# Performance work log

Measured on AMD Instinct MI355X. Metric: run time of the kernel, lower is better.

Reference implementation:

```python
import jax, jax.numpy as jnp
import numpy as np

HIDDEN = 512
LAYERS = 2
MAX_ROLLOUT = 12
STATE_SIZE = [8, 6, 4, 1]
ANCHOR = 64
BATCH = 1024
BLOCK_N = len(STATE_SIZE)


def setup_inputs() -> dict:
    key = jax.random.key(0)
    ks = jax.random.split(key, 20)
    s = 0.05
    d = {}
    d["x0"] = jax.random.normal(ks[0], (1, BATCH, HIDDEN), jnp.float32)
    d["lstm_Wih"] = jax.random.normal(ks[1], (LAYERS, 4 * HIDDEN, HIDDEN), jnp.float32) * s
    d["lstm_Whh"] = jax.random.normal(ks[2], (LAYERS, 4 * HIDDEN, HIDDEN), jnp.float32) * s
    d["lstm_bih"] = jax.random.normal(ks[3], (LAYERS, 4 * HIDDEN), jnp.float32) * s
    d["lstm_bhh"] = jax.random.normal(ks[4], (LAYERS, 4 * HIDDEN), jnp.float32) * s
    d["Wc0"] = jax.random.normal(ks[5], (STATE_SIZE[0], HIDDEN), jnp.float32) * s
    d["bc0"] = jax.random.normal(ks[6], (STATE_SIZE[0],), jnp.float32) * s
    d["Wc1"] = jax.random.normal(ks[7], (STATE_SIZE[1], HIDDEN), jnp.float32) * s
    d["bc1"] = jax.random.normal(ks[8], (STATE_SIZE[1],), jnp.float32) * s
    d["Wc2"] = jax.random.normal(ks[9], (STATE_SIZE[2], HIDDEN), jnp.float32) * s
    d["bc2"] = jax.random.normal(ks[10], (STATE_SIZE[2],), jnp.float32) * s
    d["Wprev"] = jax.random.normal(ks[11], (ANCHOR, HIDDEN), jnp.float32) * s
    d["bprev"] = jax.random.normal(ks[12], (ANCHOR,), jnp.float32) * s
    d["Wcurr"] = jax.random.normal(ks[13], (ANCHOR, HIDDEN), jnp.float32) * s
    d["bcurr"] = jax.random.normal(ks[14], (ANCHOR,), jnp.float32) * s
    d["Wanc"] = jax.random.normal(ks[15], (HIDDEN, MAX_ROLLOUT - 1), jnp.float32) * s
    d["banc"] = jax.random.normal(ks[16], (HIDDEN,), jnp.float32) * s
    d["v"] = jax.random.normal(ks[17], (ANCHOR,), jnp.float32)
    d["batch_size"] = BATCH
    return d


def _lstm_step(x, h, c, Wih, Whh, bih, bhh):
    # x: [B,H]; h,c: [L,B,H]; multi-layer LSTM, torch gate order (i,f,g,o)
    hs, cs = [], []
    inp = x
    for l in range(LAYERS):
        g = inp @ Wih[l].T + h[l] @ Whh[l].T + bih[l] + bhh[l]  # [B,4H]
        gi, gf, gg, go = jnp.split(g, 4, axis=-1)
        cl = jax.nn.sigmoid(gf) * c[l] + jax.nn.sigmoid(gi) * jnp.tanh(gg)
        hl = jax.nn.sigmoid(go) * jnp.tanh(cl)
        hs.append(hl)
        cs.append(cl)
        inp = hl
    return inp, jnp.stack(hs), jnp.stack(cs)


def _forward(x0, lstm_Wih, lstm_Whh, lstm_bih, lstm_bhh, Wc0, bc0, Wc1, bc1, Wc2, bc2,
             Wprev, bprev, Wcurr, bcurr, Wanc, banc, v, batch_size):
    Wcls = [Wc0, Wc1, Wc2]
    bcls = [bc0, bc1, bc2]
    B = batch_size
    anchor_hs = [jnp.zeros((B, HIDDEN), x0.dtype)]
    inp = x0[0]  # [B,H]
    h = jnp.zeros((LAYERS, B, HIDDEN), x0.dtype)
    c = jnp.zeros((LAYERS, B, HIDDEN), x0.dtype)
    outputs = []
    for i in range(MAX_ROLLOUT * BLOCK_N):
        state_idx = i % BLOCK_N
        cycle_idx = i // BLOCK_N
        out, h, c = _lstm_step(inp, h, c, lstm_Wih, lstm_Whh, lstm_bih, lstm_bhh)
        if state_idx < BLOCK_N - 1:
            logit = out @ Wcls[state_idx].T + bcls[state_idx]
            outputs.append(jax.nn.softmax(logit, axis=-1))  # [B, STATE_SIZE[state_idx]]
            # note: `inp` is NOT updated on classifier steps, matching the original
        else:
            anchor_hs.append(out)
            if cycle_idx == 0:
                anchor_o = jnp.zeros((B, MAX_ROLLOUT - 1), x0.dtype)
            else:
                # attention over anchor_hs[0:cycle_idx] (zeros + previous cycles),
                # exactly as the original indexes after appending current out
                prev = jnp.stack(anchor_hs[:cycle_idx])  # [cyc, B, H]
                t = jnp.tanh(prev @ Wprev.T + bprev + (out @ Wcurr.T + bcurr)[None])  # [cyc,B,A]
                scores = jax.nn.sigmoid(jnp.einsum('a,cba->cb', v, t))  # [cyc, B]
                anchor_o = jnp.pad(scores.T, ((0, 0), (0, MAX_ROLLOUT - cycle_idx - 1)))
            outputs.append(anchor_o)  # [B, MAX_ROLLOUT-1]
            inp = anchor_o @ Wanc.T + banc  # anchor_embedding feeds next step
    # outputs are [B, S_i] / [B, MAX_ROLLOUT-1]; concat into a single [B, 348] tensor
    return jnp.concatenate(outputs, axis=1)


def reference(x0, lstm_Wih, lstm_Whh, lstm_bih, lstm_bhh, Wc0, bc0, Wc1, bc1, Wc2, bc2,
              Wprev, bprev, Wcurr, bcurr, Wanc, banc, v, batch_size):
    return _forward(x0, lstm_Wih, lstm_Whh, lstm_bih, lstm_bhh, Wc0, bc0, Wc1, bc1, Wc2, bc2,
                    Wprev, bprev, Wcurr, bcurr, Wanc, banc, v, batch_size)
```

## Files before the change

kernel.cpp:

```cpp
#include <hip/hip_runtime.h>
#include <hip/hip_bf16.h>

#define BATCH 1024
#define HID   512
#define OUTW  348
#define BK    64

using short8 = __attribute__((ext_vector_type(8))) short;
using bf16x8 = __attribute__((ext_vector_type(8))) __bf16;
using f32x4  = __attribute__((ext_vector_type(4))) float;

__device__ __forceinline__ float bf2f(unsigned short u) {
  union { unsigned int i; float f; } x; x.i = ((unsigned int)u) << 16; return x.f;
}
__device__ __forceinline__ unsigned short f2bf(float f) {
  __hip_bfloat16 b = __float2bfloat16(f);
  return __builtin_bit_cast(unsigned short, b);
}
__device__ __forceinline__ float sigm(float x) { return 1.0f / (1.0f + __expf(-x)); }

__device__ __forceinline__ f32x4 mfma_bf16(short8 a, short8 b, f32x4 c) {
  return __builtin_amdgcn_mfma_f32_16x16x32_bf16(
      __builtin_bit_cast(bf16x8, a), __builtin_bit_cast(bf16x8, b), c, 0, 0, 0);
}

typedef const __attribute__((address_space(1))) unsigned int* gas_p;
typedef __attribute__((address_space(3))) unsigned int* las_p;
__device__ __forceinline__ void gload16(const void* g, void* l) {
  __builtin_amdgcn_global_load_lds((gas_p)g, (las_p)l, 16, 0, 0);
}


__global__ void k_convert(const float* __restrict__ src, unsigned short* __restrict__ dst, int n) {
  int i = (blockIdx.x * blockDim.x + threadIdx.x) * 4;
  if (i + 3 < n) {
    float4 v = *(const float4*)(src + i);
    dst[i + 0] = f2bf(v.x); dst[i + 1] = f2bf(v.y);
    dst[i + 2] = f2bf(v.z); dst[i + 3] = f2bf(v.w);
  } else {
    for (int j = 0; j < 4 && i + j < n; ++j) dst[i + j] = f2bf(src[i + j]);
  }
}

__global__ void k_wqp(const float* __restrict__ Wcurr, const float* __restrict__ Wprev,
                      unsigned short* __restrict__ dst) {
  int i = blockIdx.x * blockDim.x + threadIdx.x;
  int row = i >> 9, col = i & 511;
  float v = (row < 64) ? Wcurr[row * 512 + col] : Wprev[(row - 64) * 512 + col];
  dst[i] = f2bf(v);
}

__global__ void k_bias(const float* __restrict__ bih, const float* __restrict__ bhh,
                       float* __restrict__ bsum) {
  int i = blockIdx.x * blockDim.x + threadIdx.x;
  if (i < 4096) bsum[i] = bih[i] + bhh[i];
}

__global__ void k_zero(uint4* __restrict__ p, int n16) {
  int i = blockIdx.x * blockDim.x + threadIdx.x;
  if (i < n16) p[i] = make_uint4(0u, 0u, 0u, 0u);
}

__global__ void k_p0(float* __restrict__ P, const float* __restrict__ bprev) {
  int i = blockIdx.x * blockDim.x + threadIdx.x;
  P[i] = bprev[i & 63];
}

__global__ __launch_bounds__(256) void k_gates(
    const unsigned short* __restrict__ Xin,
    const unsigned short* __restrict__ Hprev,
    const unsigned short* __restrict__ Wih,
    const unsigned short* __restrict__ Whh,
    const float* __restrict__ bias,
    float* __restrict__ C,
    unsigned short* __restrict__ Hout)
{
  __shared__ unsigned short Ab[2][4096];
  __shared__ unsigned short Bb[2][4096];
  const int w = threadIdx.x >> 6, lane = threadIdx.x & 63;
  const int m0 = blockIdx.x * 64;
  const int n0 = blockIdx.y * 16;
  const int l16 = lane & 15, kg = lane >> 4;

  auto stage = [&](int kt, int buf) {
    const unsigned short* Asrc = (kt < 8) ? Xin : Hprev;
    const unsigned short* Wsrc = (kt < 8) ? Wih : Whh;
    const int k0 = (kt & 7) * BK;
#pragma unroll
    for (int j = 0; j < 2; ++j) {
      int s = w * 128 + j * 64 + lane;
      int row = s >> 3;
      int ke = ((s & 7) ^ (row & 7)) << 3;
      gload16(Asrc + (size_t)(m0 + row) * HID + k0 + ke, &Ab[buf][(w * 128 + j * 64) * 8]);
    }
#pragma unroll
    for (int j = 0; j < 2; ++j) {
      int s = w * 128 + j * 64 + lane;
      int fr = s >> 3;
      int g = fr >> 4, c = fr & 15;
      int ke = ((s & 7) ^ (fr & 7)) << 3;
      gload16(Wsrc + (size_t)(g * 512 + n0 + c) * HID + k0 + ke, &Bb[buf][(w * 128 + j * 64) * 8]);
    }
  };

  f32x4 acc[4];
#pragma unroll
  for (int g = 0; g < 4; ++g) acc[g] = (f32x4)(0.0f);

  stage(0, 0);
  for (int kt = 0; kt < 16; ++kt) {
    __syncthreads();
    if (kt < 15) stage(kt + 1, (kt + 1) & 1);
    const int buf = kt & 1;
#pragma unroll
    for (int ko = 0; ko < 2; ++ko) {
      const int acb = ko * 64 + kg * 16;
      const int ar = w * 16 + l16;
      short8 a = *(const short8*)&Ab[buf][ar * 64 + ((acb ^ ((ar & 7) << 4)) >> 1)];
#pragma unroll
      for (int g = 0; g < 4; ++g) {
        const int br = g * 16 + l16;
        short8 b = *(const short8*)&Bb[buf][br * 64 + ((acb ^ ((br & 7) << 4)) >> 1)];
        acc[g] = mfma_bf16(a, b, acc[g]);
      }
    }
  }

  const int ccol = n0 + l16;
  const int crow = m0 + w * 16 + kg * 4;
  const float b0 = bias[ccol], b1 = bias[512 + ccol];
  const float b2 = bias[1024 + ccol], b3 = bias[1536 + ccol];
#pragma unroll
  for (int r = 0; r < 4; ++r) {
    const int m = crow + r;
    float gi = acc[0][r] + b0;
    float gf = acc[1][r] + b1;
    float gg = acc[2][r] + b2;
    float go = acc[3][r] + b3;
    float cold = C[m * HID + ccol];
    float cn = sigm(gf) * cold + sigm(gi) * tanhf(gg);
    float hn = sigm(go) * tanhf(cn);
    C[m * HID + ccol] = cn;
    Hout[m * HID + ccol] = f2bf(hn);
  }
}

template <int S>
__global__ __launch_bounds__(256) void k_cls(const unsigned short* __restrict__ h1,
                                             const float* __restrict__ Wc,
                                             const float* __restrict__ bc,
                                             float* __restrict__ out, int obase) {
  const int wave = threadIdx.x >> 6, lane = threadIdx.x & 63;
  const int r = blockIdx.x * 4 + wave;
  short8 hv = *(const short8*)(h1 + r * HID + lane * 8);
  float hf[8];
#pragma unroll
  for (int j = 0; j < 8; ++j) hf[j] = bf2f((unsigned short)hv[j]);
  float logit[S];
#pragma unroll
  for (int s = 0; s < S; ++s) {
    const float* wr = Wc + s * HID + lane * 8;
    float p = 0.f;
#pragma unroll
    for (int j = 0; j < 8; ++j) p += hf[j] * wr[j];
#pragma unroll
    for (int off = 32; off; off >>= 1) p += __shfl_xor(p, off);
    logit[s] = p + bc[s];
  }
  if (lane == 0) {
    float m = logit[0];
#pragma unroll
    for (int s = 1; s < S; ++s) m = fmaxf(m, logit[s]);
    float e[S], den = 0.f;
#pragma unroll
    for (int s = 0; s < S; ++s) { e[s] = __expf(logit[s] - m); den += e[s]; }
    float inv = 1.0f / den;
#pragma unroll
    for (int s = 0; s < S; ++s) out[r * OUTW + obase + s] = e[s] * inv;
  }
}

__global__ __launch_bounds__(256) void k_qp(
    const unsigned short* __restrict__ h1,
    const unsigned short* __restrict__ Wqp,
    const float* __restrict__ bcurr, const float* __restrict__ bprev,
    float* __restrict__ Q,
    float* __restrict__ P,
    int cyc) {
  __shared__ unsigned short Ab[2][4096];
  __shared__ unsigned short Bb[2][1024];
  const int w = threadIdx.x >> 6, lane = threadIdx.x & 63;
  const int m0 = blockIdx.x * 64, n0 = blockIdx.y * 16;
  const int l16 = lane & 15, kg = lane >> 4;

  auto stage = [&](int kt, int buf) {
    const int k0 = kt * BK;
#pragma unroll
    for (int j = 0; j < 2; ++j) {
      int s = w * 128 + j * 64 + lane;
      int row = s >> 3;
      int ke = ((s & 7) ^ (row & 7)) << 3;
      gload16(h1 + (size_t)(m0 + row) * HID + k0 + ke, &Ab[buf][(w * 128 + j * 64) * 8]);
    }
    if (w < 2) {
      int s = w * 64 + lane;
      int row = s >> 3;
      int ke = ((s & 7) ^ (row & 7)) << 3;
      gload16(Wqp + (size_t)(n0 + row) * HID + k0 + ke, &Bb[buf][(w * 64) * 8]);
    }
  };

  f32x4 acc = (f32x4)(0.0f);
  stage(0, 0);
  for (int kt = 0; kt < 8; ++kt) {
    __syncthreads();
    if (kt < 7) stage(kt + 1, (kt + 1) & 1);
    const int buf = kt & 1;
#pragma unroll
    for (int ko = 0; ko < 2; ++ko) {
      const int acb = ko * 64 + kg * 16;
      const int ar = w * 16 + l16;
      short8 a = *(const short8*)&Ab[buf][ar * 64 + ((acb ^ ((ar & 7) << 4)) >> 1)];
      const int br = l16;
      short8 b = *(const short8*)&Bb[buf][br * 64 + ((acb ^ ((br & 7) << 4)) >> 1)];
      acc = mfma_bf16(a, b, acc);
    }
  }

  const int col = n0 + l16;
  const int r0 = m0 + w * 16 + kg * 4;
#pragma unroll
  for (int r = 0; r < 4; ++r) {
    const int m = r0 + r;
    float val = acc[r] + (col < 64 ? bcurr[col] : bprev[col - 64]);
    if (col < 64) Q[m * 64 + col] = val;
    else if (cyc + 1 < 12) P[(cyc + 1) * (BATCH * 64) + m * 64 + (col - 64)] = val;
  }
}

template <int CYC>
__global__ __launch_bounds__(256) void k_scores(
    const float* __restrict__ Q, const float* __restrict__ P,
    const float* __restrict__ vv, const float* __restrict__ Wanc,
    const float* __restrict__ banc, float* __restrict__ out,
    unsigned short* __restrict__ X) {
  const int w = threadIdx.x >> 6, lane = threadIdx.x & 63;
  const int r = blockIdx.x * 4 + w;
  const float q = Q[r * 64 + lane];
  const float vl = vv[lane];
  float sk[CYC > 0 ? CYC : 1];
#pragma unroll
  for (int k = 0; k < CYC; ++k) {
    float t = tanhf(P[k * (BATCH * 64) + r * 64 + lane] + q) * vl;
#pragma unroll
    for (int off = 32; off; off >>= 1) t += __shfl_xor(t, off);
    sk[k] = sigm(t);
  }
  float ov = 0.0f;
#pragma unroll
  for (int k = 0; k < 11; ++k)
    if (lane == k) ov = (k < CYC) ? sk[k] : 0.0f;
  if (lane < 11) out[r * OUTW + CYC * 29 + 18 + lane] = ov;

  const int d0 = lane * 8;
#pragma unroll
  for (int j = 0; j < 8; ++j) {
    const int d = d0 + j;
    float x = banc[d];
#pragma unroll
    for (int k = 0; k < CYC; ++k) x += sk[k] * Wanc[d * 11 + k];
    X[r * HID + d] = f2bf(x);
  }
}


extern "C" void kernel_launch(void* const* d_in, const int* in_sizes, int n_in,
                              void* d_out, int out_size, void* d_ws, size_t ws_size,
                              hipStream_t stream) {
  const float* x0    = (const float*)d_in[0];
  const float* lWih  = (const float*)d_in[1];
  const float* lWhh  = (const float*)d_in[2];
  const float* lbih  = (const float*)d_in[3];
  const float* lbhh  = (const float*)d_in[4];
  const float* Wc0   = (const float*)d_in[5];
  const float* bc0   = (const float*)d_in[6];
  const float* Wc1   = (const float*)d_in[7];
  const float* bc1   = (const float*)d_in[8];
  const float* Wc2   = (const float*)d_in[9];
  const float* bc2   = (const float*)d_in[10];
  const float* Wprev = (const float*)d_in[11];
  const float* bprev = (const float*)d_in[12];
  const float* Wcurr = (const float*)d_in[13];
  const float* bcurr = (const float*)d_in[14];
  const float* Wanc  = (const float*)d_in[15];
  const float* banc  = (const float*)d_in[16];
  const float* v     = (const float*)d_in[17];
  float* out = (float*)d_out;

  const size_t NW  = 2 * 2048 * 512;
  const size_t NBH = (size_t)BATCH * HID;

  char* ws = (char*)d_ws;
  size_t off = 0;
  auto alloc = [&](size_t bytes) { char* p = ws + off; off += (bytes + 255) & ~(size_t)255; return p; };
  unsigned short* Wih_b = (unsigned short*)alloc(NW * 2);
  unsigned short* Whh_b = (unsigned short*)alloc(NW * 2);
  unsigned short* Wqp_b = (unsigned short*)alloc(128 * 512 * 2);
  float*          biasS = (float*)alloc(4096 * 4);
  unsigned short* Xb    = (unsigned short*)alloc(NBH * 2);
  unsigned short* Hb0   = (unsigned short*)alloc(2 * NBH * 2);
  unsigned short* Hb1   = (unsigned short*)alloc(2 * NBH * 2);
  float*          C0    = (float*)alloc(NBH * 4);
  float*          C1    = (float*)alloc(NBH * 4);
  float*          P     = (float*)alloc((size_t)12 * BATCH * 64 * 4);
  float*          Qb    = (float*)alloc((size_t)BATCH * 64 * 4);

  k_convert<<<dim3((NW / 4 + 255) / 256), dim3(256), 0, stream>>>(lWih, Wih_b, (int)NW);
  k_convert<<<dim3((NW / 4 + 255) / 256), dim3(256), 0, stream>>>(lWhh, Whh_b, (int)NW);
  k_convert<<<dim3((NBH / 4 + 255) / 256), dim3(256), 0, stream>>>(x0, Xb, (int)NBH);
  k_wqp<<<dim3(256), dim3(256), 0, stream>>>(Wcurr, Wprev, Wqp_b);
  k_bias<<<dim3(16), dim3(256), 0, stream>>>(lbih, lbhh, biasS);
  {
    size_t zb = 2 * NBH * 2 + 2 * NBH * 2 + NBH * 4 + NBH * 4;
    int n16 = (int)(zb / 16);
    k_zero<<<dim3((n16 + 255) / 256), dim3(256), 0, stream>>>((uint4*)Hb0, n16);
  }
  k_p0<<<dim3(256), dim3(256), 0, stream>>>(P, bprev);

  for (int t = 0; t < 48; ++t) {
    const int rd = t & 1, wr = (t + 1) & 1;
    unsigned short* h0r = Hb0 + rd * NBH;
    unsigned short* h0w = Hb0 + wr * NBH;
    unsigned short* h1r = Hb1 + rd * NBH;
    unsigned short* h1w = Hb1 + wr * NBH;

    k_gates<<<dim3(16, 32), dim3(256), 0, stream>>>(Xb, h0r, Wih_b, Whh_b, biasS, C0, h0w);
    k_gates<<<dim3(16, 32), dim3(256), 0, stream>>>(h0w, h1r, Wih_b + 2048 * 512,
                                                    Whh_b + 2048 * 512, biasS + 2048, C1, h1w);
    const int st = t & 3, cyc = t >> 2, base = cyc * 29;
    if (st == 0)      k_cls<8><<<dim3(256), dim3(256), 0, stream>>>(h1w, Wc0, bc0, out, base);
    else if (st == 1) k_cls<6><<<dim3(256), dim3(256), 0, stream>>>(h1w, Wc1, bc1, out, base + 8);
    else if (st == 2) k_cls<4><<<dim3(256), dim3(256), 0, stream>>>(h1w, Wc2, bc2, out, base + 14);
    else {
      k_qp<<<dim3(16, 8), dim3(256), 0, stream>>>(h1w, Wqp_b, bcurr, bprev, Qb, P, cyc);
      switch (cyc) {
        case 0:  k_scores<0><<<dim3(256), dim3(256), 0, stream>>>(Qb, P, v, Wanc, banc, out, Xb); break;
        case 1:  k_scores<1><<<dim3(256), dim3(256), 0, stream>>>(Qb, P, v, Wanc, banc, out, Xb); break;
        case 2:  k_scores<2><<<dim3(256), dim3(256), 0, stream>>>(Qb, P, v, Wanc, banc, out, Xb); break;
        case 3:  k_scores<3><<<dim3(256), dim3(256), 0, stream>>>(Qb, P, v, Wanc, banc, out, Xb); break;
        case 4:  k_scores<4><<<dim3(256), dim3(256), 0, stream>>>(Qb, P, v, Wanc, banc, out, Xb); break;
        case 5:  k_scores<5><<<dim3(256), dim3(256), 0, stream>>>(Qb, P, v, Wanc, banc, out, Xb); break;
        case 6:  k_scores<6><<<dim3(256), dim3(256), 0, stream>>>(Qb, P, v, Wanc, banc, out, Xb); break;
        case 7:  k_scores<7><<<dim3(256), dim3(256), 0, stream>>>(Qb, P, v, Wanc, banc, out, Xb); break;
        case 8:  k_scores<8><<<dim3(256), dim3(256), 0, stream>>>(Qb, P, v, Wanc, banc, out, Xb); break;
        case 9:  k_scores<9><<<dim3(256), dim3(256), 0, stream>>>(Qb, P, v, Wanc, banc, out, Xb); break;
        case 10: k_scores<10><<<dim3(256), dim3(256), 0, stream>>>(Qb, P, v, Wanc, banc, out, Xb); break;
        default: k_scores<11><<<dim3(256), dim3(256), 0, stream>>>(Qb, P, v, Wanc, banc, out, Xb); break;
      }
    }
  }
  (void)in_sizes; (void)n_in; (void)out_size; (void)ws_size;
}
```

Baseline: 1.698 ms.

## Wavefront-fuse LSTM layer GEMMs across timesteps with larger tiles and fused classifiers

Replaces the per-layer gate kernels with a merged kernel that runs layer 1 at step t together with layer 0 at step t+1, plus the classifier head of the previous step, in one launch. The GEMM tile grows from 64x16 to 128x32 cells per block, with each wave computing a 4x4 grid of MFMA tiles, so operands are reused more per LDS load. Launch count and serialization between dependent kernels drop. The cost is fewer blocks per launch (128 per GEMM), higher register and LDS use, and more complex buffer indexing across timesteps.

```diff
diff --git a/kernel.cpp b/kernel.cpp
--- a/kernel.cpp
+++ b/kernel.cpp
@@ -4,7 +4,6 @@
 #define BATCH 1024
 #define HID   512
 #define OUTW  348
-#define BK    64
 
 using short8 = __attribute__((ext_vector_type(8))) short;
 using bf16x8 = __attribute__((ext_vector_type(8))) __bf16;
@@ -66,46 +65,55 @@
   P[i] = bprev[i & 63];
 }
 
-__global__ __launch_bounds__(256) void k_gates(
-    const unsigned short* __restrict__ Xin,
-    const unsigned short* __restrict__ Hprev,
-    const unsigned short* __restrict__ Wih,
-    const unsigned short* __restrict__ Whh,
-    const float* __restrict__ bias,
-    float* __restrict__ C,
-    unsigned short* __restrict__ Hout)
-{
-  __shared__ unsigned short Ab[2][4096];
-  __shared__ unsigned short Bb[2][4096];
-  const int w = threadIdx.x >> 6, lane = threadIdx.x & 63;
-  const int m0 = blockIdx.x * 64;
-  const int n0 = blockIdx.y * 16;
+
+struct GJob {
+  const unsigned short *X, *H, *Wih, *Whh;
+  const float *bias;
+  float *C;
+  unsigned short *Hout;
+};
+struct CJob {
+  const unsigned short* h;
+  const float *Wc, *bc;
+  float* out;
+  int obase;
+};
+
+__device__ __forceinline__ void run_gemm(const GJob& j, int lb,
+                                         unsigned short (*Ab)[8192],
+                                         unsigned short (*Bb)[8192]) {
+  const int tid = threadIdx.x, w = tid >> 6, lane = tid & 63;
+  const int wm = w & 1, wc = w >> 1;
+  const int mt = lb & 7, nt = lb >> 3;
+  const int m0 = mt * 128, n0 = nt * 32;
   const int l16 = lane & 15, kg = lane >> 4;
 
   auto stage = [&](int kt, int buf) {
-    const unsigned short* Asrc = (kt < 8) ? Xin : Hprev;
-    const unsigned short* Wsrc = (kt < 8) ? Wih : Whh;
-    const int k0 = (kt & 7) * BK;
-#pragma unroll
-    for (int j = 0; j < 2; ++j) {
-      int s = w * 128 + j * 64 + lane;
-      int row = s >> 3;
-      int ke = ((s & 7) ^ (row & 7)) << 3;
-      gload16(Asrc + (size_t)(m0 + row) * HID + k0 + ke, &Ab[buf][(w * 128 + j * 64) * 8]);
-    }
-#pragma unroll
-    for (int j = 0; j < 2; ++j) {
-      int s = w * 128 + j * 64 + lane;
-      int fr = s >> 3;
-      int g = fr >> 4, c = fr & 15;
-      int ke = ((s & 7) ^ (fr & 7)) << 3;
-      gload16(Wsrc + (size_t)(g * 512 + n0 + c) * HID + k0 + ke, &Bb[buf][(w * 128 + j * 64) * 8]);
+    const unsigned short* As = (kt < 8) ? j.X : j.H;
+    const unsigned short* Bs = (kt < 8) ? j.Wih : j.Whh;
+    const int k0 = (kt & 7) * 64;
+#pragma unroll
+    for (int i = 0; i < 4; ++i) {
+      int g = i * 256 + tid;
+      int row = g >> 3, cg = g & 7;
+      int ke = (cg ^ (row & 7)) << 3;
+      gload16(As + (size_t)(m0 + row) * HID + k0 + ke, &Ab[buf][g * 8]);
+    }
+#pragma unroll
+    for (int i = 0; i < 4; ++i) {
+      int g = i * 256 + tid;
+      int fr = g >> 3, cg = g & 7;
+      int gate = fr >> 5, cell = fr & 31;
+      int ke = (cg ^ (fr & 7)) << 3;
+      gload16(Bs + (size_t)(gate * HID + n0 + cell) * HID + k0 + ke, &Bb[buf][g * 8]);
     }
   };
 
-  f32x4 acc[4];
-#pragma unroll
-  for (int g = 0; g < 4; ++g) acc[g] = (f32x4)(0.0f);
+  f32x4 acc[4][4];
+#pragma unroll
+  for (int mi = 0; mi < 4; ++mi)
+#pragma unroll
+    for (int g = 0; g < 4; ++g) acc[mi][g] = (f32x4)(0.0f);
 
   stage(0, 0);
   for (int kt = 0; kt < 16; ++kt) {
@@ -115,68 +123,91 @@
 #pragma unroll
     for (int ko = 0; ko < 2; ++ko) {
       const int acb = ko * 64 + kg * 16;
-      const int ar = w * 16 + l16;
-      short8 a = *(const short8*)&Ab[buf][ar * 64 + ((acb ^ ((ar & 7) << 4)) >> 1)];
+      short8 a[4], b[4];
+#pragma unroll
+      for (int mi = 0; mi < 4; ++mi) {
+        const int r = wm * 64 + mi * 16 + l16;
+        a[mi] = *(const short8*)&Ab[buf][r * 64 + ((acb ^ ((r & 7) << 4)) >> 1)];
+      }
 #pragma unroll
       for (int g = 0; g < 4; ++g) {
-        const int br = g * 16 + l16;
-        short8 b = *(const short8*)&Bb[buf][br * 64 + ((acb ^ ((br & 7) << 4)) >> 1)];
-        acc[g] = mfma_bf16(a, b, acc[g]);
+        const int fr = g * 32 + wc * 16 + l16;
+        b[g] = *(const short8*)&Bb[buf][fr * 64 + ((acb ^ ((fr & 7) << 4)) >> 1)];
       }
-    }
-  }
-
-  const int ccol = n0 + l16;
-  const int crow = m0 + w * 16 + kg * 4;
-  const float b0 = bias[ccol], b1 = bias[512 + ccol];
-  const float b2 = bias[1024 + ccol], b3 = bias[1536 + ccol];
-#pragma unroll
-  for (int r = 0; r < 4; ++r) {
-    const int m = crow + r;
-    float gi = acc[0][r] + b0;
-    float gf = acc[1][r] + b1;
-    float gg = acc[2][r] + b2;
-    float go = acc[3][r] + b3;
-    float cold = C[m * HID + ccol];
-    float cn = sigm(gf) * cold + sigm(gi) * tanhf(gg);
-    float hn = sigm(go) * tanhf(cn);
-    C[m * HID + ccol] = cn;
-    Hout[m * HID + ccol] = f2bf(hn);
+#pragma unroll
+      for (int mi = 0; mi < 4; ++mi)
+#pragma unroll
+        for (int g = 0; g < 4; ++g) acc[mi][g] = mfma_bf16(a[mi], b[g], acc[mi][g]);
+    }
+  }
+
+  const int cell = n0 + wc * 16 + l16;
+  const float b0 = j.bias[cell], b1 = j.bias[512 + cell];
+  const float b2 = j.bias[1024 + cell], b3 = j.bias[1536 + cell];
+#pragma unroll
+  for (int mi = 0; mi < 4; ++mi) {
+#pragma unroll
+    for (int r = 0; r < 4; ++r) {
+      const int m = m0 + wm * 64 + mi * 16 + kg * 4 + r;
+      float gi = acc[mi][0][r] + b0;
+      float gf = acc[mi][1][r] + b1;
+      float gg = acc[mi][2][r] + b2;
+      float go = acc[mi][3][r] + b3;
+      float cold = j.C[m * HID + cell];
+      float cn = sigm(gf) * cold + sigm(gi) * tanhf(gg);
+      float hn = sigm(go) * tanhf(cn);
+      j.C[m * HID + cell] = cn;
+      j.Hout[m * HID + cell] = f2bf(hn);
+    }
   }
 }
 
 template <int S>
-__global__ __launch_bounds__(256) void k_cls(const unsigned short* __restrict__ h1,
-                                             const float* __restrict__ Wc,
-                                             const float* __restrict__ bc,
-                                             float* __restrict__ out, int obase) {
-  const int wave = threadIdx.x >> 6, lane = threadIdx.x & 63;
-  const int r = blockIdx.x * 4 + wave;
-  short8 hv = *(const short8*)(h1 + r * HID + lane * 8);
-  float hf[8];
-#pragma unroll
-  for (int j = 0; j < 8; ++j) hf[j] = bf2f((unsigned short)hv[j]);
-  float logit[S];
-#pragma unroll
-  for (int s = 0; s < S; ++s) {
-    const float* wr = Wc + s * HID + lane * 8;
-    float p = 0.f;
-#pragma unroll
-    for (int j = 0; j < 8; ++j) p += hf[j] * wr[j];
-#pragma unroll
-    for (int off = 32; off; off >>= 1) p += __shfl_xor(p, off);
-    logit[s] = p + bc[s];
-  }
-  if (lane == 0) {
-    float m = logit[0];
-#pragma unroll
-    for (int s = 1; s < S; ++s) m = fmaxf(m, logit[s]);
-    float e[S], den = 0.f;
-#pragma unroll
-    for (int s = 0; s < S; ++s) { e[s] = __expf(logit[s] - m); den += e[s]; }
-    float inv = 1.0f / den;
-#pragma unroll
-    for (int s = 0; s < S; ++s) out[r * OUTW + obase + s] = e[s] * inv;
+__device__ __forceinline__ void run_cls(const CJob& c, int cb) {
+  const int w = threadIdx.x >> 6, lane = threadIdx.x & 63;
+#pragma unroll
+  for (int i = 0; i < 8; ++i) {
+    const int r = (cb * 4 + w) * 8 + i;
+    short8 hv = *(const short8*)(c.h + r * HID + lane * 8);
+    float hf[8];
+#pragma unroll
+    for (int j = 0; j < 8; ++j) hf[j] = bf2f((unsigned short)hv[j]);
+    float logit[S];
+#pragma unroll
+    for (int s = 0; s < S; ++s) {
+      const float* wr = c.Wc + s * HID + lane * 8;
+      float p = 0.f;
+#pragma unroll
+      for (int j = 0; j < 8; ++j) p += hf[j] * wr[j];
+#pragma unroll
+      for (int off = 32; off; off >>= 1) p += __shfl_xor(p, off);
+      logit[s] = p + c.bc[s];
+    }
+    if (lane == 0) {
+      float m = logit[0];
+#pragma unroll
+      for (int s = 1; s < S; ++s) m = fmaxf(m, logit[s]);
+      float e[S], den = 0.f;
+#pragma unroll
+      for (int s = 0; s < S; ++s) { e[s] = __expf(logit[s] - m); den += e[s]; }
+      float inv = 1.0f / den;
+#pragma unroll
+      for (int s = 0; s < S; ++s) c.out[r * OUTW + c.obase + s] = e[s] * inv;
+    }
+  }
+}
+
+template <int S, bool HASB>
+__global__ __launch_bounds__(256, 2) void k_gates2(GJob A, GJob B, CJob C) {
+  __shared__ unsigned short Ab[2][8192];
+  __shared__ unsigned short Bb[2][8192];
+  const int b = blockIdx.x;
+  if (b < 128) {
+    run_gemm(A, b, Ab, Bb);
+  } else if (HASB && b < 256) {
+    run_gemm(B, b - 128, Ab, Bb);
+  } else {
+    if constexpr (S > 0) run_cls<S>(C, b - (HASB ? 256 : 128));
   }
 }
 
@@ -194,7 +225,7 @@
   const int l16 = lane & 15, kg = lane >> 4;
 
   auto stage = [&](int kt, int buf) {
-    const int k0 = kt * BK;
+    const int k0 = kt * 64;
 #pragma unroll
     for (int j = 0; j < 2; ++j) {
       int s = w * 128 + j * 64 + lane;
@@ -327,37 +358,50 @@
   }
   k_p0<<<dim3(256), dim3(256), 0, stream>>>(P, bprev);
 
-  for (int t = 0; t < 48; ++t) {
-    const int rd = t & 1, wr = (t + 1) & 1;
-    unsigned short* h0r = Hb0 + rd * NBH;
-    unsigned short* h0w = Hb0 + wr * NBH;
-    unsigned short* h1r = Hb1 + rd * NBH;
-    unsigned short* h1w = Hb1 + wr * NBH;
-
-    k_gates<<<dim3(16, 32), dim3(256), 0, stream>>>(Xb, h0r, Wih_b, Whh_b, biasS, C0, h0w);
-    k_gates<<<dim3(16, 32), dim3(256), 0, stream>>>(h0w, h1r, Wih_b + 2048 * 512,
-                                                    Whh_b + 2048 * 512, biasS + 2048, C1, h1w);
-    const int st = t & 3, cyc = t >> 2, base = cyc * 29;
-    if (st == 0)      k_cls<8><<<dim3(256), dim3(256), 0, stream>>>(h1w, Wc0, bc0, out, base);
-    else if (st == 1) k_cls<6><<<dim3(256), dim3(256), 0, stream>>>(h1w, Wc1, bc1, out, base + 8);
-    else if (st == 2) k_cls<4><<<dim3(256), dim3(256), 0, stream>>>(h1w, Wc2, bc2, out, base + 14);
-    else {
-      k_qp<<<dim3(16, 8), dim3(256), 0, stream>>>(h1w, Wqp_b, bcurr, bprev, Qb, P, cyc);
-      switch (cyc) {
-        case 0:  k_scores<0><<<dim3(256), dim3(256), 0, stream>>>(Qb, P, v, Wanc, banc, out, Xb); break;
-        case 1:  k_scores<1><<<dim3(256), dim3(256), 0, stream>>>(Qb, P, v, Wanc, banc, out, Xb); break;
-        case 2:  k_scores<2><<<dim3(256), dim3(256), 0, stream>>>(Qb, P, v, Wanc, banc, out, Xb); break;
-        case 3:  k_scores<3><<<dim3(256), dim3(256), 0, stream>>>(Qb, P, v, Wanc, banc, out, Xb); break;
-        case 4:  k_scores<4><<<dim3(256), dim3(256), 0, stream>>>(Qb, P, v, Wanc, banc, out, Xb); break;
-        case 5:  k_scores<5><<<dim3(256), dim3(256), 0, stream>>>(Qb, P, v, Wanc, banc, out, Xb); break;
-        case 6:  k_scores<6><<<dim3(256), dim3(256), 0, stream>>>(Qb, P, v, Wanc, banc, out, Xb); break;
-        case 7:  k_scores<7><<<dim3(256), dim3(256), 0, stream>>>(Qb, P, v, Wanc, banc, out, Xb); break;
-        case 8:  k_scores<8><<<dim3(256), dim3(256), 0, stream>>>(Qb, P, v, Wanc, banc, out, Xb); break;
-        case 9:  k_scores<9><<<dim3(256), dim3(256), 0, stream>>>(Qb, P, v, Wanc, banc, out, Xb); break;
-        case 10: k_scores<10><<<dim3(256), dim3(256), 0, stream>>>(Qb, P, v, Wanc, banc, out, Xb); break;
-        default: k_scores<11><<<dim3(256), dim3(256), 0, stream>>>(Qb, P, v, Wanc, banc, out, Xb); break;
-      }
-    }
+  auto jobL0 = [&](int u) {
+    GJob j; j.X = Xb; j.H = Hb0 + (u & 1) * NBH;
+    j.Wih = Wih_b; j.Whh = Whh_b; j.bias = biasS; j.C = C0;
+    j.Hout = Hb0 + ((u + 1) & 1) * NBH; return j;
+  };
+  auto jobL1 = [&](int t) {
+    GJob j; j.X = Hb0 + ((t + 1) & 1) * NBH; j.H = Hb1 + (t & 1) * NBH;
+    j.Wih = Wih_b + 2048 * 512; j.Whh = Whh_b + 2048 * 512; j.bias = biasS + 2048; j.C = C1;
+    j.Hout = Hb1 + ((t + 1) & 1) * NBH; return j;
+  };
+  auto h1of = [&](int t) { return (const unsigned short*)(Hb1 + ((t + 1) & 1) * NBH); };
+  GJob dummy{}; CJob nocls{};
+
+  k_gates2<0, false><<<dim3(128), dim3(256), 0, stream>>>(jobL0(0), dummy, nocls);
+
+  for (int c = 0; c < 12; ++c) {
+    const int t0 = 4 * c, t1 = t0 + 1, t2 = t0 + 2, t3 = t0 + 3;
+    const int base = c * 29;
+    CJob cls0{h1of(t0), Wc0, bc0, out, base};
+    CJob cls1{h1of(t1), Wc1, bc1, out, base + 8};
+    CJob cls2{h1of(t2), Wc2, bc2, out, base + 14};
+
+    k_gates2<0, true><<<dim3(256), dim3(256), 0, stream>>>(jobL1(t0), jobL0(t1), nocls);
+    k_gates2<8, true><<<dim3(288), dim3(256), 0, stream>>>(jobL1(t1), jobL0(t2), cls0);
+    k_gates2<6, true><<<dim3(288), dim3(256), 0, stream>>>(jobL1(t2), jobL0(t3), cls1);
+    k_gates2<4, false><<<dim3(160), dim3(256), 0, stream>>>(jobL1(t3), dummy, cls2);
+
+    k_qp<<<dim3(16, 8), dim3(256), 0, stream>>>(h1of(t3), Wqp_b, bcurr, bprev, Qb, P, c);
+    switch (c) {
+      case 0:  k_scores<0><<<dim3(256), dim3(256), 0, stream>>>(Qb, P, v, Wanc, banc, out, Xb); break;
+      case 1:  k_scores<1><<<dim3(256), dim3(256), 0, stream>>>(Qb, P, v, Wanc, banc, out, Xb); break;
+      case 2:  k_scores<2><<<dim3(256), dim3(256), 0, stream>>>(Qb, P, v, Wanc, banc, out, Xb); break;
+      case 3:  k_scores<3><<<dim3(256), dim3(256), 0, stream>>>(Qb, P, v, Wanc, banc, out, Xb); break;
+      case 4:  k_scores<4><<<dim3(256), dim3(256), 0, stream>>>(Qb, P, v, Wanc, banc, out, Xb); break;
+      case 5:  k_scores<5><<<dim3(256), dim3(256), 0, stream>>>(Qb, P, v, Wanc, banc, out, Xb); break;
+      case 6:  k_scores<6><<<dim3(256), dim3(256), 0, stream>>>(Qb, P, v, Wanc, banc, out, Xb); break;
+      case 7:  k_scores<7><<<dim3(256), dim3(256), 0, stream>>>(Qb, P, v, Wanc, banc, out, Xb); break;
+      case 8:  k_scores<8><<<dim3(256), dim3(256), 0, stream>>>(Qb, P, v, Wanc, banc, out, Xb); break;
+      case 9:  k_scores<9><<<dim3(256), dim3(256), 0, stream>>>(Qb, P, v, Wanc, banc, out, Xb); break;
+      case 10: k_scores<10><<<dim3(256), dim3(256), 0, stream>>>(Qb, P, v, Wanc, banc, out, Xb); break;
+      default: k_scores<11><<<dim3(256), dim3(256), 0, stream>>>(Qb, P, v, Wanc, banc, out, Xb); break;
+    }
+    if (c < 11)
+      k_gates2<0, false><<<dim3(128), dim3(256), 0, stream>>>(jobL0(t3 + 1), dummy, nocls);
   }
   (void)in_sizes; (void)n_in; (void)out_size; (void)ws_size;
 }
```

After: 2.623 ms. 1.54x slower.
